# Kernel tuning notes

Measured on AMD Instinct MI355X. Metric: run time of the kernel, lower is better.

## Reference

```python
import jax, jax.numpy as jnp
import numpy as np

N_EMB = 1024
N_HEAD = 16
EPS = 1e-5


def _linear_params(key, fan_in, fan_out):
    k1, k2 = jax.random.split(key)
    lim = 1.0 / np.sqrt(fan_in)
    W = jax.random.uniform(k1, (fan_in, fan_out), minval=-lim, maxval=lim, dtype=jnp.float32)
    b = jax.random.uniform(k2, (fan_out,), minval=-lim, maxval=lim, dtype=jnp.float32)
    return W, b


def setup_inputs() -> dict:
    key = jax.random.key(0)
    ks = jax.random.split(key, 8)
    x = jax.random.normal(ks[0], (4, 2048, N_EMB), dtype=jnp.float32)
    Wk, bk = _linear_params(ks[1], N_EMB, N_EMB)
    Wq, bq = _linear_params(ks[2], N_EMB, N_EMB)
    Wv, bv = _linear_params(ks[3], N_EMB, N_EMB)
    Wp, bp = _linear_params(ks[4], N_EMB, N_EMB)
    W1, b1 = _linear_params(ks[5], N_EMB, 4 * N_EMB)
    W2, b2 = _linear_params(ks[6], 4 * N_EMB, N_EMB)
    return {
        "x": x,
        "ln1_g": jnp.ones((N_EMB,), jnp.float32), "ln1_b": jnp.zeros((N_EMB,), jnp.float32),
        "Wk": Wk, "bk": bk, "Wq": Wq, "bq": bq, "Wv": Wv, "bv": bv, "Wp": Wp, "bp": bp,
        "ln2_g": jnp.ones((N_EMB,), jnp.float32), "ln2_b": jnp.zeros((N_EMB,), jnp.float32),
        "W1": W1, "b1": b1, "W2": W2, "b2": b2,
        "cond_len": 256,
    }


def _layernorm(x, g, b):
    mu = jnp.mean(x, axis=-1, keepdims=True)
    var = jnp.mean(jnp.square(x - mu), axis=-1, keepdims=True)
    return (x - mu) * jax.lax.rsqrt(var + EPS) * g + b


def _hybrid_mask(T, cond_len):
    # rows attend to all conditioning columns; causal within the remaining block
    i = jnp.arange(T)[:, None]
    j = jnp.arange(T)[None, :]
    return (j < cond_len) | ((i >= cond_len) & (j >= cond_len) & (j <= i))  # [T,T] bool


def _block(x, ln1_g, ln1_b, Wk, bk, Wq, bq, Wv, bv, Wp, bp, ln2_g, ln2_b, W1, b1, W2, b2, cond_len):
    B, T, C = x.shape
    hd = C // N_HEAD
    h = _layernorm(x, ln1_g, ln1_b)
    # QKV: [B,T,C] -> [B,H,T,hd]
    q = (h @ Wq + bq).reshape(B, T, N_HEAD, hd).transpose(0, 2, 1, 3)
    k = (h @ Wk + bk).reshape(B, T, N_HEAD, hd).transpose(0, 2, 1, 3)
    v = (h @ Wv + bv).reshape(B, T, N_HEAD, hd).transpose(0, 2, 1, 3)
    att = jnp.einsum('bhqd,bhkd->bhqk', q, k) * (1.0 / np.sqrt(hd))
    mask = _hybrid_mask(T, cond_len)
    att = jnp.where(mask, att, -jnp.inf)
    att = jax.nn.softmax(att, axis=-1)
    y = jnp.einsum('bhqk,bhkd->bhqd', att, v)
    y = y.transpose(0, 2, 1, 3).reshape(B, T, C)
    x = x + (y @ Wp + bp)
    h2 = _layernorm(x, ln2_g, ln2_b)
    m = jax.nn.gelu(h2 @ W1 + b1, approximate=False) @ W2 + b2
    return x + m


def reference(x, ln1_g, ln1_b, Wk, bk, Wq, bq, Wv, bv, Wp, bp, ln2_g, ln2_b, W1, b1, W2, b2, cond_len):
    return _block(x, ln1_g, ln1_b, Wk, bk, Wq, bq, Wv, bv, Wp, bp, ln2_g, ln2_b, W1, b1, W2, b2, cond_len)
```

## Files before the change

### kernel.cpp

```cpp
#include <hip/hip_runtime.h>

typedef __bf16 bf16;
typedef __attribute__((ext_vector_type(4))) __bf16 bf16x4;
typedef __attribute__((ext_vector_type(8))) __bf16 bf16x8;
typedef __attribute__((ext_vector_type(4))) float f32x4;

__global__ __launch_bounds__(256)
void transpose_f32_bf16(const float* __restrict__ src, bf16* __restrict__ dst, int R, int C)
{
  __shared__ bf16 tile[32][33];
  const int tx = threadIdx.x & 31, ty = threadIdx.x >> 5;
  const int c0 = blockIdx.x * 32, r0 = blockIdx.y * 32;
#pragma unroll
  for (int i = 0; i < 4; ++i)
    tile[ty + i * 8][tx] = (bf16)src[(size_t)(r0 + ty + i * 8) * C + c0 + tx];
  __syncthreads();
#pragma unroll
  for (int i = 0; i < 4; ++i)
    dst[(size_t)(c0 + ty + i * 8) * R + r0 + tx] = tile[tx][ty + i * 8];
}

__global__ __launch_bounds__(256)
void ln_f32_bf16(const float* __restrict__ x, const float* __restrict__ g,
                 const float* __restrict__ bta, bf16* __restrict__ out)
{
  const int row = blockIdx.x * 4 + (threadIdx.x >> 6);
  const int l = threadIdx.x & 63;
  const float* xr = x + (size_t)row * 1024 + l * 16;
  f32x4 a[4];
#pragma unroll
  for (int i = 0; i < 4; ++i) a[i] = ((const f32x4*)xr)[i];
  float s = 0.f, s2 = 0.f;
#pragma unroll
  for (int i = 0; i < 4; ++i)
#pragma unroll
    for (int jj = 0; jj < 4; ++jj) { float vv = a[i][jj]; s += vv; s2 += vv * vv; }
#pragma unroll
  for (int m = 1; m < 64; m <<= 1) { s += __shfl_xor(s, m); s2 += __shfl_xor(s2, m); }
  const float mu = s * (1.0f / 1024.0f);
  const float var = s2 * (1.0f / 1024.0f) - mu * mu;
  const float rs = rsqrtf(var + 1e-5f);
  f32x4 gv[4], bv[4];
#pragma unroll
  for (int i = 0; i < 4; ++i) {
    gv[i] = ((const f32x4*)(g + l * 16))[i];
    bv[i] = ((const f32x4*)(bta + l * 16))[i];
  }
  bf16x8 o0, o1;
#pragma unroll
  for (int i = 0; i < 8; ++i) {
    float v0 = a[i >> 2][i & 3];
    float v1 = a[2 + (i >> 2)][i & 3];
    o0[i] = (bf16)((v0 - mu) * rs * gv[i >> 2][i & 3] + bv[i >> 2][i & 3]);
    o1[i] = (bf16)((v1 - mu) * rs * gv[2 + (i >> 2)][i & 3] + bv[2 + (i >> 2)][i & 3]);
  }
  bf16* orow = out + (size_t)row * 1024 + l * 16;
  ((bf16x8*)orow)[0] = o0;
  ((bf16x8*)orow)[1] = o1;
}

template <int EPI>
__global__ __launch_bounds__(256)
void gemm_bt(const bf16* __restrict__ A, const bf16* __restrict__ Bt,
             const float* __restrict__ bias, void* __restrict__ out,
             const float* __restrict__ res, int M, int N, int K, float oscale)
{
  __shared__ bf16 As[128 * 40];
  __shared__ bf16 Bs[128 * 40];
  const int tid = threadIdx.x;
  const int l = tid & 63;
  const int w = tid >> 6;
  const int wm = w >> 1, wn = w & 1;
  const int m0 = blockIdx.x * 128;
  const int n0 = blockIdx.y * 128;

  const int r0 = tid >> 2;
  const int s0 = (tid & 3) * 8;

  const bf16* ga0 = A + (size_t)(m0 + r0) * K + s0;
  const bf16* ga1 = A + (size_t)(m0 + 64 + r0) * K + s0;
  const bf16* gb0 = Bt + (size_t)(n0 + r0) * K + s0;
  const bf16* gb1 = Bt + (size_t)(n0 + 64 + r0) * K + s0;

  f32x4 acc[4][4] = {};
  bf16x8 ra0 = *(const bf16x8*)ga0;
  bf16x8 ra1 = *(const bf16x8*)ga1;
  bf16x8 rb0 = *(const bf16x8*)gb0;
  bf16x8 rb1 = *(const bf16x8*)gb1;

  const int KT = K >> 5;
  const int lrow = l & 15;
  const int lslot = (l >> 4) * 8;

  for (int kt = 0; kt < KT; ++kt) {
    __syncthreads();
    *(bf16x8*)&As[(r0)      * 40 + s0] = ra0;
    *(bf16x8*)&As[(r0 + 64) * 40 + s0] = ra1;
    *(bf16x8*)&Bs[(r0)      * 40 + s0] = rb0;
    *(bf16x8*)&Bs[(r0 + 64) * 40 + s0] = rb1;
    __syncthreads();
    if (kt + 1 < KT) {
      const int ko = (kt + 1) * 32;
      ra0 = *(const bf16x8*)(ga0 + ko);
      ra1 = *(const bf16x8*)(ga1 + ko);
      rb0 = *(const bf16x8*)(gb0 + ko);
      rb1 = *(const bf16x8*)(gb1 + ko);
    }
    bf16x8 af[4], bfv[4];
#pragma unroll
    for (int i = 0; i < 4; ++i)
      af[i] = *(const bf16x8*)&As[(wm * 64 + i * 16 + lrow) * 40 + lslot];
#pragma unroll
    for (int i = 0; i < 4; ++i)
      bfv[i] = *(const bf16x8*)&Bs[(wn * 64 + i * 16 + lrow) * 40 + lslot];
#pragma unroll
    for (int mi = 0; mi < 4; ++mi)
#pragma unroll
      for (int ni = 0; ni < 4; ++ni)
        acc[mi][ni] = __builtin_amdgcn_mfma_f32_16x16x32_bf16(af[mi], bfv[ni], acc[mi][ni], 0, 0, 0);
  }

#pragma unroll
  for (int mi = 0; mi < 4; ++mi) {
#pragma unroll
    for (int ni = 0; ni < 4; ++ni) {
      const int col = n0 + wn * 64 + ni * 16 + (l & 15);
      const float bv = bias[col];
#pragma unroll
      for (int j = 0; j < 4; ++j) {
        const int row = m0 + wm * 64 + mi * 16 + (l >> 4) * 4 + j;
        float val = acc[mi][ni][j] + bv;
        if constexpr (EPI == 1) {
          const int b = row >> 11, t = row & 2047, hh = col >> 6, d = col & 63;
          ((bf16*)out)[(((size_t)(b * 16 + hh) * 2048 + t) * 64) + d] = (bf16)(val * oscale);
        } else if constexpr (EPI == 2) {
          const int b = row >> 11, t = row & 2047, hh = col >> 6, d = col & 63;
          ((bf16*)out)[(((size_t)(b * 16 + hh) * 64 + d) * 2048) + t] = (bf16)val;
        } else if constexpr (EPI == 3) {
          ((float*)out)[(size_t)row * 1024 + col] = val + res[(size_t)row * 1024 + col];
        } else if constexpr (EPI == 4) {
          const float ge = 0.5f * val * (1.0f + erff(val * 0.70710678118f));
          ((bf16*)out)[(size_t)row * N + col] = (bf16)ge;
        } else if constexpr (EPI == 5) {
          ((float*)out)[(size_t)row * 1024 + col] = val + res[(size_t)row * 1024 + col];
        }
      }
    }
  }
}

__global__ __launch_bounds__(512)
void attn_kernel(const bf16* __restrict__ q, const bf16* __restrict__ k,
                 const bf16* __restrict__ v, bf16* __restrict__ y,
                 const int* __restrict__ condp)
{
  __shared__ bf16 Ks[2][64 * 72];
  __shared__ bf16 Vs[2][64 * 72];
  __shared__ char PsB[8][2048];
  const int tid = threadIdx.x, l = tid & 63, w = tid >> 6;
  const int bx = blockIdx.x;
  const int qt = 15 - (bx >> 6);
  const int bh = bx & 63;
  const int bb = bh >> 4, hh = bh & 15;
  const int cond = condp[0];
  const int iLo = qt * 128;
  const size_t base = (size_t)bh * 2048 * 64;

  const int lrow = l & 15;
  const int g = l >> 4;
  const int lslot = g * 8;

  const int qrow = iLo + w * 16 + lrow;
  const bf16x8 bq0 = *(const bf16x8*)(q + base + (size_t)qrow * 64 + lslot);
  const bf16x8 bq1 = *(const bf16x8*)(q + base + (size_t)qrow * 64 + 32 + lslot);

  f32x4 o[4] = {};
  float m = -1e30f, lsum = 0.f;

  const int ckt = (cond + 63) >> 6;
  int nkt = ((iLo + 127) >> 6) + 1;
  if (nkt < ckt) nkt = ckt;
  const int wHi = iLo + w * 16 + 15;

  const int kr = tid >> 3;
  const int ks8 = (tid & 7) * 8;
  const bf16* kp = k + base + (size_t)kr * 64 + ks8;
  const bf16* vp = v + base + (size_t)kr * 2048 + ks8;

  bf16x8 rk = *(const bf16x8*)kp;
  bf16x8 rv = *(const bf16x8*)vp;
  *(bf16x8*)&Ks[0][kr * 72 + ks8] = rk;
  *(bf16x8*)&Vs[0][kr * 72 + ks8] = rv;
  __syncthreads();

  char* psw = PsB[w];

  for (int kt = 0; kt < nkt; ++kt) {
    const int cur = kt & 1;
    const int j0 = kt << 6;
    const bool pf = (kt + 1 < nkt);
    if (pf) {
      rk = *(const bf16x8*)(kp + (size_t)(j0 + 64) * 64);
      rv = *(const bf16x8*)(vp + j0 + 64);
    }

    const bool active = (j0 < cond) || (j0 <= wHi);
    if (active) {
      f32x4 sfr[4];
      __builtin_amdgcn_s_setprio(1);
#pragma unroll
      for (int nf = 0; nf < 4; ++nf) {
        f32x4 s = {};
        bf16x8 ka0 = *(const bf16x8*)&Ks[cur][(nf * 16 + lrow) * 72 + lslot];
        bf16x8 ka1 = *(const bf16x8*)&Ks[cur][(nf * 16 + lrow) * 72 + 32 + lslot];
        s = __builtin_amdgcn_mfma_f32_16x16x32_bf16(ka0, bq0, s, 0, 0, 0);
        s = __builtin_amdgcn_mfma_f32_16x16x32_bf16(ka1, bq1, s, 0, 0, 0);
        sfr[nf] = s;
      }
      __builtin_amdgcn_s_setprio(0);

      const bool safe = (j0 + 63 < cond) || (j0 + 63 <= iLo + w * 16);
      if (!safe) {
#pragma unroll
        for (int nf = 0; nf < 4; ++nf)
#pragma unroll
          for (int j = 0; j < 4; ++j) {
            const int kc = j0 + nf * 16 + g * 4 + j;
            const bool ok = (kc < cond) || (kc <= qrow);
            sfr[nf][j] = ok ? sfr[nf][j] : -1e30f;
          }
      }

      float pmax = sfr[0][0];
#pragma unroll
      for (int nf = 0; nf < 4; ++nf)
#pragma unroll
        for (int j = 0; j < 4; ++j) pmax = fmaxf(pmax, sfr[nf][j]);
      pmax = fmaxf(pmax, __shfl_xor(pmax, 16));
      pmax = fmaxf(pmax, __shfl_xor(pmax, 32));

      const bool resc = !__all(pmax - m <= 8.0f);
      if (resc) {
        const float mnew = fmaxf(m, pmax);
        const float alpha = __expf(m - mnew);
        m = mnew;
        lsum *= alpha;
        float ar[4];
#pragma unroll
        for (int j = 0; j < 4; ++j) ar[j] = __shfl(alpha, (l & 48) | (g * 4 + j));
#pragma unroll
        for (int df = 0; df < 4; ++df)
#pragma unroll
          for (int j = 0; j < 4; ++j) o[df][j] *= ar[j];
      }

      float rsum = 0.f;
#pragma unroll
      for (int nf = 0; nf < 4; ++nf) {
        bf16x4 pk;
#pragma unroll
        for (int j = 0; j < 4; ++j) {
          const float p = __expf(sfr[nf][j] - m);
          rsum += p;
          pk[j] = (bf16)p;
        }
        const int slot = 2 * nf + (g >> 1);
        const int boff = lrow * 128 + ((slot ^ (lrow & 7)) << 4) + (g & 1) * 8;
        *(bf16x4*)(psw + boff) = pk;
      }
      rsum += __shfl_xor(rsum, 16);
      rsum += __shfl_xor(rsum, 32);
      lsum += rsum;

      const int r0b = lrow * 128 + (((g    ) ^ (lrow & 7)) << 4);
      const int r1b = lrow * 128 + (((g + 4) ^ (lrow & 7)) << 4);
      const bf16x8 pa0 = *(const bf16x8*)(psw + r0b);
      const bf16x8 pa1 = *(const bf16x8*)(psw + r1b);
      __builtin_amdgcn_s_setprio(1);
#pragma unroll
      for (int df = 0; df < 4; ++df) {
        bf16x8 v0 = *(const bf16x8*)&Vs[cur][(df * 16 + lrow) * 72 + lslot];
        bf16x8 v1 = *(const bf16x8*)&Vs[cur][(df * 16 + lrow) * 72 + 32 + lslot];
        o[df] = __builtin_amdgcn_mfma_f32_16x16x32_bf16(pa0, v0, o[df], 0, 0, 0);
        o[df] = __builtin_amdgcn_mfma_f32_16x16x32_bf16(pa1, v1, o[df], 0, 0, 0);
      }
      __builtin_amdgcn_s_setprio(0);
    }

    if (pf) {
      *(bf16x8*)&Ks[cur ^ 1][kr * 72 + ks8] = rk;
      *(bf16x8*)&Vs[cur ^ 1][kr * 72 + ks8] = rv;
    }
    __syncthreads();
  }

  float lr[4];
#pragma unroll
  for (int j = 0; j < 4; ++j) lr[j] = 1.0f / __shfl(lsum, (l & 48) | (g * 4 + j));
#pragma unroll
  for (int df = 0; df < 4; ++df)
#pragma unroll
    for (int j = 0; j < 4; ++j) {
      const int irow = iLo + w * 16 + g * 4 + j;
      y[((size_t)bb * 2048 + irow) * 1024 + hh * 64 + df * 16 + lrow] = (bf16)(o[df][j] * lr[j]);
    }
}

extern "C" void kernel_launch(void* const* d_in, const int* in_sizes, int n_in,
                              void* d_out, int out_size, void* d_ws, size_t ws_size,
                              hipStream_t stream) {
  const float* x    = (const float*)d_in[0];
  const float* ln1g = (const float*)d_in[1];
  const float* ln1b = (const float*)d_in[2];
  const float* Wk   = (const float*)d_in[3];
  const float* bk   = (const float*)d_in[4];
  const float* Wq   = (const float*)d_in[5];
  const float* bq   = (const float*)d_in[6];
  const float* Wv   = (const float*)d_in[7];
  const float* bv   = (const float*)d_in[8];
  const float* Wp   = (const float*)d_in[9];
  const float* bpb  = (const float*)d_in[10];
  const float* ln2g = (const float*)d_in[11];
  const float* ln2b = (const float*)d_in[12];
  const float* W1   = (const float*)d_in[13];
  const float* b1   = (const float*)d_in[14];
  const float* W2   = (const float*)d_in[15];
  const float* b2   = (const float*)d_in[16];
  const int*  cond  = (const int*)d_in[17];
  float* out = (float*)d_out;

  char* ws = (char*)d_ws;
  const size_t MB = 1024ull * 1024ull;
  if (ws_size < 136 * MB) return;

  bf16*  WqT  = (bf16*)(ws + 0 * MB);
  bf16*  WkT  = (bf16*)(ws + 2 * MB);
  bf16*  WvT  = (bf16*)(ws + 4 * MB);
  bf16*  WpT  = (bf16*)(ws + 6 * MB);
  bf16*  W1T  = (bf16*)(ws + 8 * MB);
  bf16*  W2T  = (bf16*)(ws + 16 * MB);
  float* x2   = (float*)(ws + 24 * MB);
  bf16*  hbuf = (bf16*)(ws + 56 * MB);
  bf16*  qb   = (bf16*)(ws + 72 * MB);
  bf16*  kb   = (bf16*)(ws + 88 * MB);
  bf16*  vb   = (bf16*)(ws + 104 * MB);
  bf16*  yb   = (bf16*)(ws + 120 * MB);
  bf16*  m1   = (bf16*)(ws + 72 * MB);

  dim3 blk(256);
  transpose_f32_bf16<<<dim3(32, 32), blk, 0, stream>>>(Wq, WqT, 1024, 1024);
  transpose_f32_bf16<<<dim3(32, 32), blk, 0, stream>>>(Wk, WkT, 1024, 1024);
  transpose_f32_bf16<<<dim3(32, 32), blk, 0, stream>>>(Wv, WvT, 1024, 1024);
  transpose_f32_bf16<<<dim3(32, 32), blk, 0, stream>>>(Wp, WpT, 1024, 1024);
  transpose_f32_bf16<<<dim3(128, 32), blk, 0, stream>>>(W1, W1T, 1024, 4096);
  transpose_f32_bf16<<<dim3(32, 128), blk, 0, stream>>>(W2, W2T, 4096, 1024);

  ln_f32_bf16<<<2048, blk, 0, stream>>>(x, ln1g, ln1b, hbuf);

  gemm_bt<1><<<dim3(64, 8), blk, 0, stream>>>(hbuf, WqT, bq, qb, nullptr, 8192, 1024, 1024, 0.125f);
  gemm_bt<1><<<dim3(64, 8), blk, 0, stream>>>(hbuf, WkT, bk, kb, nullptr, 8192, 1024, 1024, 1.0f);
  gemm_bt<2><<<dim3(64, 8), blk, 0, stream>>>(hbuf, WvT, bv, vb, nullptr, 8192, 1024, 1024, 1.0f);

  attn_kernel<<<dim3(1024), dim3(512), 0, stream>>>(qb, kb, vb, yb, cond);

  gemm_bt<3><<<dim3(64, 8), blk, 0, stream>>>(yb, WpT, bpb, x2, x, 8192, 1024, 1024, 1.0f);
  ln_f32_bf16<<<2048, blk, 0, stream>>>(x2, ln2g, ln2b, hbuf);
  gemm_bt<4><<<dim3(64, 32), blk, 0, stream>>>(hbuf, W1T, b1, m1, nullptr, 8192, 4096, 1024, 1.0f);
  gemm_bt<5><<<dim3(64, 8), blk, 0, stream>>>(m1, W2T, b2, out, x2, 8192, 1024, 4096, 1.0f);
}
```

Baseline: 418.5 us.

## Use direct global-to-LDS double-buffered loads, XCD block remap, and fused QKV GEMM

The GEMM kernel now stages A and B tiles straight into LDS with global_load_lds into two buffers. The next tile's load is issued before the current tile's MFMAs, which removes the register round-trip and one barrier per k-step. Blocks are remapped so neighbouring tiles land on the same XCD chiplet, for better L2 reuse. The Q, K and V projections are merged into one N=3072 GEMM over a concatenated transposed weight, with per-segment bias and output routing in the epilogue. In exchange, the LDS rows lose their padding, which may cause bank conflicts, and correctness relies on the async LDS writes being properly waited on before the barrier.

```diff
diff --git a/kernel.cpp b/kernel.cpp
--- a/kernel.cpp
+++ b/kernel.cpp
@@ -4,6 +4,12 @@
 typedef __attribute__((ext_vector_type(4))) __bf16 bf16x4;
 typedef __attribute__((ext_vector_type(8))) __bf16 bf16x8;
 typedef __attribute__((ext_vector_type(4))) float f32x4;
+
+__device__ __forceinline__ void stage16(const bf16* g, bf16* l) {
+  __builtin_amdgcn_global_load_lds(
+      (const __attribute__((address_space(1))) void*)g,
+      (__attribute__((address_space(3))) void*)l, 16, 0, 0);
+}
 
 __global__ __launch_bounds__(256)
 void transpose_f32_bf16(const float* __restrict__ src, bf16* __restrict__ dst, int R, int C)
@@ -62,80 +68,89 @@
 template <int EPI>
 __global__ __launch_bounds__(256)
 void gemm_bt(const bf16* __restrict__ A, const bf16* __restrict__ Bt,
-             const float* __restrict__ bias, void* __restrict__ out,
-             const float* __restrict__ res, int M, int N, int K, float oscale)
+             const float* __restrict__ bias, const float* __restrict__ biasK,
+             const float* __restrict__ biasV,
+             void* __restrict__ out, void* __restrict__ outK, void* __restrict__ outV,
+             const float* __restrict__ res, int M, int N, int K)
 {
-  __shared__ bf16 As[128 * 40];
-  __shared__ bf16 Bs[128 * 40];
+  __shared__ bf16 As[2][128 * 32];
+  __shared__ bf16 Bs[2][128 * 32];
   const int tid = threadIdx.x;
   const int l = tid & 63;
   const int w = tid >> 6;
   const int wm = w >> 1, wn = w & 1;
-  const int m0 = blockIdx.x * 128;
-  const int n0 = blockIdx.y * 128;
-
-  const int r0 = tid >> 2;
-  const int s0 = (tid & 3) * 8;
-
-  const bf16* ga0 = A + (size_t)(m0 + r0) * K + s0;
-  const bf16* ga1 = A + (size_t)(m0 + 64 + r0) * K + s0;
-  const bf16* gb0 = Bt + (size_t)(n0 + r0) * K + s0;
-  const bf16* gb1 = Bt + (size_t)(n0 + 64 + r0) * K + s0;
+
+  const unsigned nbx = gridDim.x;
+  const unsigned nwg = nbx * gridDim.y;
+  unsigned bid = blockIdx.x + blockIdx.y * nbx;
+  const unsigned cpx = nwg >> 3;
+  bid = (bid & 7) * cpx + (bid >> 3);
+  const int m0 = (int)(bid % nbx) * 128;
+  const int n0 = (int)(bid / nbx) * 128;
+
+  const int srow = tid >> 2;
+  const int sslot = (tid & 3) * 8;
+  const bf16* gA = A + (size_t)(m0 + srow) * K + sslot;
+  const bf16* gB = Bt + (size_t)(n0 + srow) * K + sslot;
+  const int ldsOff = srow * 32 + sslot;
+
+  const int lrow = l & 15;
+  const int lsl8 = (l >> 4) * 8;
 
   f32x4 acc[4][4] = {};
-  bf16x8 ra0 = *(const bf16x8*)ga0;
-  bf16x8 ra1 = *(const bf16x8*)ga1;
-  bf16x8 rb0 = *(const bf16x8*)gb0;
-  bf16x8 rb1 = *(const bf16x8*)gb1;
-
   const int KT = K >> 5;
-  const int lrow = l & 15;
-  const int lslot = (l >> 4) * 8;
+
+#define STAGE(buf, k0)                                        \
+  do {                                                        \
+    stage16(gA + (k0), &As[buf][ldsOff]);                     \
+    stage16(gA + (size_t)64 * K + (k0), &As[buf][2048 + ldsOff]); \
+    stage16(gB + (k0), &Bs[buf][ldsOff]);                     \
+    stage16(gB + (size_t)64 * K + (k0), &Bs[buf][2048 + ldsOff]); \
+  } while (0)
+
+  STAGE(0, 0);
+  __syncthreads();
 
   for (int kt = 0; kt < KT; ++kt) {
-    __syncthreads();
-    *(bf16x8*)&As[(r0)      * 40 + s0] = ra0;
-    *(bf16x8*)&As[(r0 + 64) * 40 + s0] = ra1;
-    *(bf16x8*)&Bs[(r0)      * 40 + s0] = rb0;
-    *(bf16x8*)&Bs[(r0 + 64) * 40 + s0] = rb1;
-    __syncthreads();
-    if (kt + 1 < KT) {
-      const int ko = (kt + 1) * 32;
-      ra0 = *(const bf16x8*)(ga0 + ko);
-      ra1 = *(const bf16x8*)(ga1 + ko);
-      rb0 = *(const bf16x8*)(gb0 + ko);
-      rb1 = *(const bf16x8*)(gb1 + ko);
-    }
+    const int cur = kt & 1;
+    if (kt + 1 < KT) STAGE(cur ^ 1, (kt + 1) << 5);
     bf16x8 af[4], bfv[4];
 #pragma unroll
     for (int i = 0; i < 4; ++i)
-      af[i] = *(const bf16x8*)&As[(wm * 64 + i * 16 + lrow) * 40 + lslot];
+      af[i] = *(const bf16x8*)&As[cur][(wm * 64 + i * 16 + lrow) * 32 + lsl8];
 #pragma unroll
     for (int i = 0; i < 4; ++i)
-      bfv[i] = *(const bf16x8*)&Bs[(wn * 64 + i * 16 + lrow) * 40 + lslot];
+      bfv[i] = *(const bf16x8*)&Bs[cur][(wn * 64 + i * 16 + lrow) * 32 + lsl8];
 #pragma unroll
     for (int mi = 0; mi < 4; ++mi)
 #pragma unroll
       for (int ni = 0; ni < 4; ++ni)
         acc[mi][ni] = __builtin_amdgcn_mfma_f32_16x16x32_bf16(af[mi], bfv[ni], acc[mi][ni], 0, 0, 0);
-  }
-
+    __syncthreads();
+  }
+#undef STAGE
+
+  const int seg = n0 >> 10;
+  const float* bp = (EPI == 0) ? (seg == 0 ? bias : (seg == 1 ? biasK : biasV)) : bias;
 #pragma unroll
   for (int mi = 0; mi < 4; ++mi) {
 #pragma unroll
     for (int ni = 0; ni < 4; ++ni) {
-      const int col = n0 + wn * 64 + ni * 16 + (l & 15);
-      const float bv = bias[col];
+      const int colg = n0 + wn * 64 + ni * 16 + lrow;
+      const int col = (EPI == 0) ? (colg & 1023) : colg;
+      const float bv = bp[col];
 #pragma unroll
       for (int j = 0; j < 4; ++j) {
         const int row = m0 + wm * 64 + mi * 16 + (l >> 4) * 4 + j;
         float val = acc[mi][ni][j] + bv;
-        if constexpr (EPI == 1) {
+        if constexpr (EPI == 0) {
           const int b = row >> 11, t = row & 2047, hh = col >> 6, d = col & 63;
-          ((bf16*)out)[(((size_t)(b * 16 + hh) * 2048 + t) * 64) + d] = (bf16)(val * oscale);
-        } else if constexpr (EPI == 2) {
-          const int b = row >> 11, t = row & 2047, hh = col >> 6, d = col & 63;
-          ((bf16*)out)[(((size_t)(b * 16 + hh) * 64 + d) * 2048) + t] = (bf16)val;
+          if (seg == 0)
+            ((bf16*)out)[(((size_t)(b * 16 + hh) * 2048 + t) * 64) + d] = (bf16)(val * 0.125f);
+          else if (seg == 1)
+            ((bf16*)outK)[(((size_t)(b * 16 + hh) * 2048 + t) * 64) + d] = (bf16)val;
+          else
+            ((bf16*)outV)[(((size_t)(b * 16 + hh) * 64 + d) * 2048) + t] = (bf16)val;
         } else if constexpr (EPI == 3) {
           ((float*)out)[(size_t)row * 1024 + col] = val + res[(size_t)row * 1024 + col];
         } else if constexpr (EPI == 4) {
@@ -272,7 +287,7 @@
       rsum += __shfl_xor(rsum, 32);
       lsum += rsum;
 
-      const int r0b = lrow * 128 + (((g    ) ^ (lrow & 7)) << 4);
+      const int r0b = lrow * 128 + (((g) ^ (lrow & 7)) << 4);
       const int r1b = lrow * 128 + (((g + 4) ^ (lrow & 7)) << 4);
       const bf16x8 pa0 = *(const bf16x8*)(psw + r0b);
       const bf16x8 pa1 = *(const bf16x8*)(psw + r1b);
@@ -333,38 +348,38 @@
   const size_t MB = 1024ull * 1024ull;
   if (ws_size < 136 * MB) return;
 
-  bf16*  WqT  = (bf16*)(ws + 0 * MB);
-  bf16*  WkT  = (bf16*)(ws + 2 * MB);
-  bf16*  WvT  = (bf16*)(ws + 4 * MB);
-  bf16*  WpT  = (bf16*)(ws + 6 * MB);
-  bf16*  W1T  = (bf16*)(ws + 8 * MB);
-  bf16*  W2T  = (bf16*)(ws + 16 * MB);
-  float* x2   = (float*)(ws + 24 * MB);
-  bf16*  hbuf = (bf16*)(ws + 56 * MB);
-  bf16*  qb   = (bf16*)(ws + 72 * MB);
-  bf16*  kb   = (bf16*)(ws + 88 * MB);
-  bf16*  vb   = (bf16*)(ws + 104 * MB);
-  bf16*  yb   = (bf16*)(ws + 120 * MB);
-  bf16*  m1   = (bf16*)(ws + 72 * MB);
+  bf16*  WqkvT = (bf16*)(ws + 0 * MB);
+  bf16*  WpT   = (bf16*)(ws + 6 * MB);
+  bf16*  W1T   = (bf16*)(ws + 8 * MB);
+  bf16*  W2T   = (bf16*)(ws + 16 * MB);
+  float* x2    = (float*)(ws + 24 * MB);
+  bf16*  hbuf  = (bf16*)(ws + 56 * MB);
+  bf16*  qb    = (bf16*)(ws + 72 * MB);
+  bf16*  kb    = (bf16*)(ws + 88 * MB);
+  bf16*  vb    = (bf16*)(ws + 104 * MB);
+  bf16*  yb    = (bf16*)(ws + 120 * MB);
+  bf16*  m1    = (bf16*)(ws + 72 * MB);
 
   dim3 blk(256);
-  transpose_f32_bf16<<<dim3(32, 32), blk, 0, stream>>>(Wq, WqT, 1024, 1024);
-  transpose_f32_bf16<<<dim3(32, 32), blk, 0, stream>>>(Wk, WkT, 1024, 1024);
-  transpose_f32_bf16<<<dim3(32, 32), blk, 0, stream>>>(Wv, WvT, 1024, 1024);
+  transpose_f32_bf16<<<dim3(32, 32), blk, 0, stream>>>(Wq, WqkvT,                1024, 1024);
+  transpose_f32_bf16<<<dim3(32, 32), blk, 0, stream>>>(Wk, WqkvT + 1024 * 1024,  1024, 1024);
+  transpose_f32_bf16<<<dim3(32, 32), blk, 0, stream>>>(Wv, WqkvT + 2048 * 1024,  1024, 1024);
   transpose_f32_bf16<<<dim3(32, 32), blk, 0, stream>>>(Wp, WpT, 1024, 1024);
   transpose_f32_bf16<<<dim3(128, 32), blk, 0, stream>>>(W1, W1T, 1024, 4096);
   transpose_f32_bf16<<<dim3(32, 128), blk, 0, stream>>>(W2, W2T, 4096, 1024);
 
   ln_f32_bf16<<<2048, blk, 0, stream>>>(x, ln1g, ln1b, hbuf);
 
-  gemm_bt<1><<<dim3(64, 8), blk, 0, stream>>>(hbuf, WqT, bq, qb, nullptr, 8192, 1024, 1024, 0.125f);
-  gemm_bt<1><<<dim3(64, 8), blk, 0, stream>>>(hbuf, WkT, bk, kb, nullptr, 8192, 1024, 1024, 1.0f);
-  gemm_bt<2><<<dim3(64, 8), blk, 0, stream>>>(hbuf, WvT, bv, vb, nullptr, 8192, 1024, 1024, 1.0f);
+  gemm_bt<0><<<dim3(64, 24), blk, 0, stream>>>(hbuf, WqkvT, bq, bk, bv,
+                                               qb, kb, vb, nullptr, 8192, 3072, 1024);
 
   attn_kernel<<<dim3(1024), dim3(512), 0, stream>>>(qb, kb, vb, yb, cond);
 
-  gemm_bt<3><<<dim3(64, 8), blk, 0, stream>>>(yb, WpT, bpb, x2, x, 8192, 1024, 1024, 1.0f);
+  gemm_bt<3><<<dim3(64, 8), blk, 0, stream>>>(yb, WpT, bpb, nullptr, nullptr,
+                                              x2, nullptr, nullptr, x, 8192, 1024, 1024);
   ln_f32_bf16<<<2048, blk, 0, stream>>>(x2, ln2g, ln2b, hbuf);
-  gemm_bt<4><<<dim3(64, 32), blk, 0, stream>>>(hbuf, W1T, b1, m1, nullptr, 8192, 4096, 1024, 1.0f);
-  gemm_bt<5><<<dim3(64, 8), blk, 0, stream>>>(m1, W2T, b2, out, x2, 8192, 1024, 4096, 1.0f);
-}
+  gemm_bt<4><<<dim3(64, 32), blk, 0, stream>>>(hbuf, W1T, b1, nullptr, nullptr,
+                                               m1, nullptr, nullptr, nullptr, 8192, 4096, 1024);
+  gemm_bt<5><<<dim3(64, 8), blk, 0, stream>>>(m1, W2T, b2, nullptr, nullptr,
+                                              out, nullptr, nullptr, x2, 8192, 1024, 4096);
+}
```

New measurement: 457.0 us. 1.09x slower.
